# Optimization experiments

Measured on AMD Instinct MI355X. Metric: run time of the kernel, lower is better.

Reference implementation:

```python
import jax, jax.numpy as jnp
import numpy as np

NUM_HEADS = 12
TOP_K = 2
ROPE_THETA = 10000.0
EPS = 1e-6

def _rmsnorm(x, w):
    return x * jax.lax.rsqrt(jnp.mean(x * x, axis=-1, keepdims=True) + EPS) * w

def _rotate_half(t):
    t1, t2 = jnp.split(t, 2, axis=-1)
    return jnp.concatenate([-t2, t1], axis=-1)

def setup_inputs() -> dict:
    key = jax.random.key(0)
    ks = jax.random.split(key, 8)
    B, S, H, E, F = 2, 2048, 768, 8, 3072
    s = 0.02
    return {
        "x": jax.random.normal(ks[0], (B, S, H), dtype=jnp.float32),
        "attn_norm_w": jnp.ones((H,), dtype=jnp.float32),
        "wqkv": jax.random.normal(ks[1], (H, 3 * H), dtype=jnp.float32) * s,
        "wo": jax.random.normal(ks[2], (H, H), dtype=jnp.float32) * s,
        "ffn_norm_w": jnp.ones((H,), dtype=jnp.float32),
        "router_w": jax.random.normal(ks[3], (H, E), dtype=jnp.float32) * s,
        "w1": jax.random.normal(ks[4], (E, H, F), dtype=jnp.float32) * s,
        "w2": jax.random.normal(ks[5], (E, F, H), dtype=jnp.float32) * s,
    }

def reference(x, attn_norm_w, wqkv, wo, ffn_norm_w, router_w, w1, w2):
    B, S, H = x.shape
    NH, Dh = NUM_HEADS, H // NUM_HEADS
    E = router_w.shape[1]

    # ---- attention sub-block: x = x + attn(rmsnorm(x)) ----
    h = _rmsnorm(x, attn_norm_w)
    qkv = h @ wqkv  # (B,S,3H)
    q, k, v = [t.reshape(B, S, NH, Dh) for t in jnp.split(qkv, 3, axis=-1)]

    # RoPE (llama-style half-split rotation)
    half = Dh // 2
    inv_freq = 1.0 / (ROPE_THETA ** (jnp.arange(half, dtype=jnp.float32) / half))
    ang = jnp.arange(S, dtype=jnp.float32)[:, None] * inv_freq[None, :]  # (S, half)
    cos = jnp.concatenate([jnp.cos(ang)] * 2, axis=-1)[None, :, None, :].astype(x.dtype)
    sin = jnp.concatenate([jnp.sin(ang)] * 2, axis=-1)[None, :, None, :].astype(x.dtype)
    q = q * cos + _rotate_half(q) * sin
    k = k * cos + _rotate_half(k) * sin

    scores = jnp.einsum('bqhd,bkhd->bhqk', q, k) / jnp.sqrt(jnp.asarray(Dh, x.dtype))
    causal = jnp.tril(jnp.ones((S, S), dtype=bool))
    scores = jnp.where(causal[None, None], scores, jnp.asarray(-1e9, x.dtype))
    attn = jax.nn.softmax(scores, axis=-1)
    o = jnp.einsum('bhqk,bkhd->bqhd', attn, v).reshape(B, S, H) @ wo
    x = x + o

    # ---- MoE FFN sub-block: x = x + moe(rmsnorm(x)) ----
    hn = _rmsnorm(x, ffn_norm_w).reshape(-1, H)  # (T,H)
    logits = hn @ router_w  # (T,E)
    probs = jax.nn.softmax(logits, axis=-1)
    top_v, top_i = jax.lax.top_k(probs, TOP_K)  # (T,K)
    top_v = top_v / jnp.sum(top_v, axis=-1, keepdims=True)
    onehot = jax.nn.one_hot(top_i, E, dtype=x.dtype)  # (T,K,E)
    combine = jnp.einsum('tke,tk->te', onehot, top_v)  # (T,E)

    h1 = jnp.einsum('th,ehf->etf', hn, w1)
    h2 = jnp.einsum('etf,efh->eth', jax.nn.silu(h1), w2)
    moe_out = jnp.einsum('eth,te->th', h2, combine).reshape(B, S, H)

    # load-balancing aux loss (switch-style)
    frac = jnp.mean(jnp.sum(onehot, axis=1), axis=0) / TOP_K  # (E,)
    mean_prob = jnp.mean(probs, axis=0)  # (E,)
    aux = jnp.asarray(E, x.dtype) * jnp.sum(frac * mean_prob)

    return (x + moe_out, aux)
```

## Files before the change

kernel.cpp:

```cpp
#include <hip/hip_runtime.h>
#include <cstdint>
#include <cstddef>

typedef __bf16 bf16;
typedef bf16 bf16x8 __attribute__((ext_vector_type(8)));
typedef bf16 bf16x4 __attribute__((ext_vector_type(4)));
typedef float f32x4 __attribute__((ext_vector_type(4)));

static constexpr size_t SKS = (size_t)10240 * 768;

template <int N> struct ICst { static constexpr int v = N; };

__device__ __forceinline__ void async_cp16(const void* g, void* l) {
    __builtin_amdgcn_global_load_lds(
        (const __attribute__((address_space(1))) unsigned int*)(unsigned long long)g,
        (__attribute__((address_space(3))) unsigned int*)(unsigned int)(unsigned long long)l,
        16, 0, 0);
}

#define BARX() __builtin_amdgcn_s_barrier()
#define LGKM0() asm volatile("s_waitcnt lgkmcnt(0)" ::: "memory")
#define VMC8() asm volatile("s_waitcnt vmcnt(8)" ::: "memory")
#define VMC0() asm volatile("s_waitcnt vmcnt(0)" ::: "memory")

template <bool NT>
__device__ __forceinline__ void tc_body(const float* __restrict__ in, bf16* __restrict__ out,
                                        int R, int C, int r0, int c0, float* shf) {
    float (*tile)[33] = (float(*)[33])shf;
    int tid = threadIdx.x;
    int lr = tid >> 3, lc = (tid & 7) * 4;
    const f32x4* gp = (const f32x4*)&in[(size_t)(r0 + lr) * C + c0 + lc];
    f32x4 v = NT ? __builtin_nontemporal_load(gp) : *gp;
    tile[lr][lc] = v[0]; tile[lr][lc + 1] = v[1]; tile[lr][lc + 2] = v[2]; tile[lr][lc + 3] = v[3];
    __syncthreads();
    int sc = tid >> 3, sr = (tid & 7) * 4;
    bf16x4 o;
    o[0] = (bf16)tile[sr][sc]; o[1] = (bf16)tile[sr + 1][sc];
    o[2] = (bf16)tile[sr + 2][sc]; o[3] = (bf16)tile[sr + 3][sc];
    bf16* dst = &out[(size_t)(c0 + sc) * R + r0 + sr];
    if (NT) {
        union { bf16x4 b; unsigned long long u; } cv;
        cv.b = o;
        __builtin_nontemporal_store(cv.u, (unsigned long long*)dst);
    } else {
        *(bf16x4*)dst = o;
    }
}

__global__ __launch_bounds__(256) void prep1(const float* __restrict__ x,
                                             const float* __restrict__ anw,
                                             bf16* __restrict__ hbuf,
                                             const float* __restrict__ wqkv,
                                             bf16* __restrict__ wqkvT,
                                             const float* __restrict__ wo,
                                             bf16* __restrict__ woT,
                                             int* __restrict__ ctrl) {
    __shared__ __align__(16) float shf[32 * 33];
    const int bid = (int)blockIdx.x, tid = threadIdx.x;
    if (bid < 4096) {
        const float* xr = x + (size_t)bid * 768;
        float v0 = xr[tid], v1 = xr[tid + 256], v2 = xr[tid + 512];
        float s = v0 * v0 + v1 * v1 + v2 * v2;
#pragma unroll
        for (int off = 32; off; off >>= 1) s += __shfl_xor(s, off, 64);
        if ((tid & 63) == 0) shf[tid >> 6] = s;
        __syncthreads();
        float tot = shf[0] + shf[1] + shf[2] + shf[3];
        float rs = rsqrtf(tot * (1.f / 768.f) + 1e-6f);
        bf16* o = hbuf + (size_t)bid * 768;
        o[tid]       = (bf16)(v0 * rs * anw[tid]);
        o[tid + 256] = (bf16)(v1 * rs * anw[tid + 256]);
        o[tid + 512] = (bf16)(v2 * rs * anw[tid + 512]);
    } else if (bid < 5824) {
        int i = bid - 4096;
        tc_body<false>(wqkv, wqkvT, 768, 2304, (i / 72) * 32, (i % 72) * 32, shf);
    } else if (bid < 6400) {
        int i = bid - 5824;
        tc_body<false>(wo, woT, 768, 768, (i / 24) * 32, (i % 24) * 32, shf);
    } else {
        if (tid < 64) ctrl[tid] = 0;
    }
}

__global__ __launch_bounds__(256) void rope_kernel(const bf16* __restrict__ qkv,
                                                   bf16* __restrict__ qb,
                                                   bf16* __restrict__ kb,
                                                   bf16* __restrict__ vtb) {
    __shared__ float vs[64][65];
    const int tid = threadIdx.x;
    const int s0 = blockIdx.x * 64, bh = blockIdx.y;
    const int b = bh / 12, h = bh - b * 12;
    const float qscale = 0.18033688f;
#pragma unroll
    for (int i = 0; i < 16; ++i) {
        int idx = i * 256 + tid;
        int sl = idx >> 6, d = idx & 63;
        int sg = s0 + sl;
        size_t base = ((size_t)b * 2048 + sg) * 2304;
        float qv = (float)qkv[base + h * 64 + d];
        float kv = (float)qkv[base + 768 + h * 64 + d];
        float vv = (float)qkv[base + 1536 + h * 64 + d];
        float qp = (float)qkv[base + h * 64 + (d ^ 32)];
        float kp = (float)qkv[base + 768 + h * 64 + (d ^ 32)];
        int jj = d & 31;
        float invf = __expf(-(float)jj * (9.210340371976184f / 32.f));
        float ang = (float)sg * invf;
        float cv, sv;
        __sincosf(ang, &sv, &cv);
        float rq = (d < 32) ? -qp : qp;
        float rk = (d < 32) ? -kp : kp;
        qb[((size_t)bh * 2048 + sg) * 64 + d] = (bf16)((qv * cv + rq * sv) * qscale);
        kb[((size_t)bh * 2048 + sg) * 64 + d] = (bf16)(kv * cv + rk * sv);
        vs[sl][d] = vv;
    }
    __syncthreads();
#pragma unroll
    for (int i = 0; i < 16; ++i) {
        int idx = i * 256 + tid;
        int d = idx >> 6, sl = idx & 63;
        vtb[(size_t)bh * 64 * 2048 + (size_t)d * 2048 + s0 + sl] = (bf16)vs[sl][d];
    }
}

struct AttnSh {
    bf16 Qs[2][64][32];
    bf16 Ks[2][2][64][32];
    bf16 Vts[2][2][64][32];
    bf16 Ps[4][1024];
};
union ShU { AttnSh a; float tile[32 * 33]; };

__global__ __launch_bounds__(256) void attn_tw(const bf16* __restrict__ qb,
                                               const bf16* __restrict__ kb,
                                               const bf16* __restrict__ vtb,
                                               bf16* __restrict__ ob,
                                               const float* __restrict__ w1,
                                               bf16* __restrict__ w1T,
                                               const float* __restrict__ w2,
                                               bf16* __restrict__ w2T) {
    __shared__ __align__(16) ShU sh;
    const int bid = (int)blockIdx.x;

    if (bid >= 768) {
        int i = bid - 768;
        if (i < 18432) {
            int bz = i / 2304, r = i - bz * 2304;
            tc_body<true>(w1 + (size_t)bz * 768 * 3072, w1T + (size_t)bz * 768 * 3072,
                          768, 3072, ((r / 96) % 24) * 32, (r % 96) * 32, sh.tile);
        } else {
            i -= 18432;
            int bz = i / 2304, r = i - bz * 2304;
            tc_body<true>(w2 + (size_t)bz * 3072 * 768, w2T + (size_t)bz * 3072 * 768,
                          3072, 768, ((r / 24) % 96) * 32, (r % 24) * 32, sh.tile);
        }
        return;
    }

    __builtin_amdgcn_s_setprio(1);

    const int tid = threadIdx.x, lane = tid & 63, w = tid >> 6;
    const int quad = lane >> 4, l16 = lane & 15;
    const int linear = bid;
    const int xcd = linear & 7, j = linear >> 3;
    const int bh = xcd * 3 + (j >> 5);
    const int qt = 31 - (j & 31);
    const int q0 = qt * 64;
    const int b = bh / 12, h = bh - b * 12;

    const bf16* qhead = qb + (size_t)bh * 2048 * 64;
    const bf16* khead = kb + (size_t)bh * 2048 * 64;
    const bf16* vthead = vtb + (size_t)bh * 64 * 2048;

#pragma unroll
    for (int i = 0; i < 2; ++i) {
        int o = (i * 256 + tid) * 16;
        int kk = o >> 12, row = (o >> 6) & 63, el = (o & 63) >> 1;
        async_cp16(qhead + (size_t)(q0 + row) * 64 + kk * 32 + el,
                   (char*)sh.a.Qs + (size_t)(i * 256 + w * 64) * 16);
    }
    __syncthreads();
    bf16x8 bq[2];
#pragma unroll
    for (int kk = 0; kk < 2; ++kk)
        bq[kk] = *(const bf16x8*)&sh.a.Qs[kk][w * 16 + l16][quad * 8];

    f32x4 o_acc[4] = {};
    float m_st = -1e30f, l_st = 0.f;

    for (int j2 = 0; j2 <= qt; j2 += 2) {
        int nt2 = (j2 + 1 <= qt) ? 2 : 1;
        __syncthreads();
#pragma unroll
        for (int t = 0; t < 2; ++t) {
            if (t >= nt2) break;
            int kv0 = (j2 + t) * 64;
#pragma unroll
            for (int i = 0; i < 2; ++i) {
                int o = (i * 256 + tid) * 16;
                int kk = o >> 12, row = (o >> 6) & 63, el = (o & 63) >> 1;
                async_cp16(khead + (size_t)(kv0 + row) * 64 + kk * 32 + el,
                           (char*)&sh.a.Ks[t] + (size_t)(i * 256 + w * 64) * 16);
                async_cp16(vthead + (size_t)row * 2048 + kv0 + kk * 32 + el,
                           (char*)&sh.a.Vts[t] + (size_t)(i * 256 + w * 64) * 16);
            }
        }
        __syncthreads();

#pragma unroll
        for (int t = 0; t < 2; ++t) {
            if (t >= nt2) break;

            f32x4 sacc[4] = {};
#pragma unroll
            for (int kk = 0; kk < 2; ++kk) {
                bf16x8 ak[4];
#pragma unroll
                for (int ni = 0; ni < 4; ++ni)
                    ak[ni] = *(const bf16x8*)&sh.a.Ks[t][kk][ni * 16 + l16][quad * 8];
#pragma unroll
                for (int ni = 0; ni < 4; ++ni)
                    sacc[ni] = __builtin_amdgcn_mfma_f32_16x16x32_bf16(ak[ni], bq[kk], sacc[ni], 0, 0, 0);
            }

            if (j2 + t == qt) {
                int ql = w * 16 + l16;
#pragma unroll
                for (int ni = 0; ni < 4; ++ni)
#pragma unroll
                    for (int r = 0; r < 4; ++r)
                        if (ni * 16 + quad * 4 + r > ql) sacc[ni][r] = -1e30f;
            }

            float mx = sacc[0][0];
#pragma unroll
            for (int ni = 0; ni < 4; ++ni)
#pragma unroll
                for (int r = 0; r < 4; ++r) mx = fmaxf(mx, sacc[ni][r]);
            mx = fmaxf(mx, __shfl_xor(mx, 16, 64));
            mx = fmaxf(mx, __shfl_xor(mx, 32, 64));
            float mnew = fmaxf(m_st, mx);
            float alpha = exp2f(m_st - mnew);
            m_st = mnew;
            float rsum = 0.f;
#pragma unroll
            for (int ni = 0; ni < 4; ++ni)
#pragma unroll
                for (int r = 0; r < 4; ++r) {
                    float pv = exp2f(sacc[ni][r] - mnew);
                    sacc[ni][r] = pv;
                    rsum += pv;
                }
            rsum += __shfl_xor(rsum, 16, 64);
            rsum += __shfl_xor(rsum, 32, 64);
            l_st = l_st * alpha + rsum;

            float af[4];
#pragma unroll
            for (int r = 0; r < 4; ++r) af[r] = __shfl(alpha, quad * 4 + r, 64);
#pragma unroll
            for (int ni = 0; ni < 4; ++ni)
#pragma unroll
                for (int r = 0; r < 4; ++r) o_acc[ni][r] *= af[r];

            bf16* pb = sh.a.Ps[w];
#pragma unroll
            for (int ni = 0; ni < 4; ++ni)
#pragma unroll
                for (int r = 0; r < 4; ++r) {
                    int kv = ni * 16 + quad * 4 + r;
                    int ch = (kv >> 3) ^ (l16 & 7);
                    pb[l16 * 64 + ch * 8 + (kv & 7)] = (bf16)sacc[ni][r];
                }

#pragma unroll
            for (int kk = 0; kk < 2; ++kk) {
                int ch = (kk * 4 + quad) ^ (l16 & 7);
                bf16x8 ap = *(const bf16x8*)&pb[l16 * 64 + ch * 8];
                bf16x8 bv[4];
#pragma unroll
                for (int ni = 0; ni < 4; ++ni)
                    bv[ni] = *(const bf16x8*)&sh.a.Vts[t][kk][ni * 16 + l16][quad * 8];
#pragma unroll
                for (int ni = 0; ni < 4; ++ni)
                    o_acc[ni] = __builtin_amdgcn_mfma_f32_16x16x32_bf16(ap, bv[ni], o_acc[ni], 0, 0, 0);
            }
        }
    }

    float lf[4];
#pragma unroll
    for (int r = 0; r < 4; ++r) lf[r] = 1.f / __shfl(l_st, quad * 4 + r, 64);
#pragma unroll
    for (int ni = 0; ni < 4; ++ni)
#pragma unroll
        for (int r = 0; r < 4; ++r) {
            int rowg = q0 + w * 16 + quad * 4 + r;
            size_t tk = (size_t)b * 2048 + rowg;
            ob[tk * 768 + h * 64 + ni * 16 + l16] = (bf16)(o_acc[ni][r] * lf[r]);
        }
    __builtin_amdgcn_s_setprio(0);
}

__global__ __launch_bounds__(256) void rms_router(const float* __restrict__ x1,
                                                  const float* __restrict__ w,
                                                  const float* __restrict__ rw,
                                                  bf16* __restrict__ hn,
                                                  int* __restrict__ topi,
                                                  float* __restrict__ topw,
                                                  float* __restrict__ probsb) {
    __shared__ float hnf[768];
    __shared__ float part[256];
    __shared__ float lg[8];
    __shared__ float probs[8];
    __shared__ float red[4];
    int row = blockIdx.x, tid = threadIdx.x;
    const float* xr = x1 + (size_t)row * 768;
    float v0 = xr[tid], v1 = xr[tid + 256], v2 = xr[tid + 512];
    float s = v0 * v0 + v1 * v1 + v2 * v2;
#pragma unroll
    for (int off = 32; off; off >>= 1) s += __shfl_xor(s, off, 64);
    if ((tid & 63) == 0) red[tid >> 6] = s;
    __syncthreads();
    float tot = red[0] + red[1] + red[2] + red[3];
    float rs = rsqrtf(tot * (1.f / 768.f) + 1e-6f);
    float h0 = v0 * rs * w[tid], h1v = v1 * rs * w[tid + 256], h2v = v2 * rs * w[tid + 512];
    hnf[tid] = h0; hnf[tid + 256] = h1v; hnf[tid + 512] = h2v;
    bf16* o = hn + (size_t)row * 768;
    o[tid] = (bf16)h0; o[tid + 256] = (bf16)h1v; o[tid + 512] = (bf16)h2v;
    __syncthreads();
    int e = tid & 7, seg = tid >> 3;
    float p = 0.f;
#pragma unroll
    for (int j = 0; j < 24; ++j) { int k = seg * 24 + j; p += hnf[k] * rw[k * 8 + e]; }
    part[tid] = p;
    __syncthreads();
    if (tid < 8) { float a = 0.f; for (int sgi = 0; sgi < 32; ++sgi) a += part[sgi * 8 + tid]; lg[tid] = a; }
    __syncthreads();
    if (tid == 0) {
        float mx = lg[0];
        for (int i = 1; i < 8; ++i) mx = fmaxf(mx, lg[i]);
        float ssum = 0.f, ex[8];
        for (int i = 0; i < 8; ++i) { ex[i] = __expf(lg[i] - mx); ssum += ex[i]; }
        float inv = 1.f / ssum;
        for (int i = 0; i < 8; ++i) probs[i] = ex[i] * inv;
        int e0 = 0; float p0 = probs[0];
        for (int i = 1; i < 8; ++i) if (probs[i] > p0) { p0 = probs[i]; e0 = i; }
        int e1 = -1; float p1 = -1.f;
        for (int i = 0; i < 8; ++i) if (i != e0 && probs[i] > p1) { p1 = probs[i]; e1 = i; }
        float wsum = p0 + p1;
        topi[row * 2] = e0; topi[row * 2 + 1] = e1;
        topw[row * 2] = p0 / wsum; topw[row * 2 + 1] = p1 / wsum;
    }
    __syncthreads();
    if (tid < 8) probsb[(size_t)row * 8 + tid] = probs[tid];
}

__global__ __launch_bounds__(256) void router_stats(const float* __restrict__ probsb,
                                                    const int* __restrict__ topi,
                                                    int* ctrl, int4* tiles, float* auxOut) {
    __shared__ float pws[4][8];
    __shared__ int cws[4][8];
    int tid = threadIdx.x;
    float s[8] = {};
    int cnt[8] = {};
    for (int t = tid; t < 4096; t += 256) {
        const float4* p = (const float4*)(probsb + (size_t)t * 8);
        float4 a = p[0], b = p[1];
        s[0] += a.x; s[1] += a.y; s[2] += a.z; s[3] += a.w;
        s[4] += b.x; s[5] += b.y; s[6] += b.z; s[7] += b.w;
        int e0 = topi[2 * t], e1 = topi[2 * t + 1];
#pragma unroll
        for (int e = 0; e < 8; ++e) cnt[e] += (e == e0) + (e == e1);
    }
#pragma unroll
    for (int e = 0; e < 8; ++e)
#pragma unroll
        for (int off = 32; off; off >>= 1) {
            s[e] += __shfl_xor(s[e], off, 64);
            cnt[e] += __shfl_xor(cnt[e], off, 64);
        }
    if ((tid & 63) == 0) {
#pragma unroll
        for (int e = 0; e < 8; ++e) { pws[tid >> 6][e] = s[e]; cws[tid >> 6][e] = cnt[e]; }
    }
    __syncthreads();
    if (tid == 0) {
        int off = 0, nt = 0;
        float aux = 0.f;
        for (int e = 0; e < 8; ++e) {
            int ne = cws[0][e] + cws[1][e] + cws[2][e] + cws[3][e];
            float ps = pws[0][e] + pws[1][e] + pws[2][e] + pws[3][e];
            ctrl[e] = ne;
            ctrl[32 + e] = off;
            int ntl = (ne + 255) >> 8;
            for (int i = 0; i < ntl; ++i) { tiles[nt] = make_int4(e, off + i * 256, off + ne, 0); ++nt; }
            off += ntl << 8;
            aux += ((float)ne * (1.f / 8192.f)) * (ps * (1.f / 4096.f));
        }
        ctrl[24] = nt;
        auxOut[0] = 8.f * aux;
    }
}

__global__ __launch_bounds__(256) void place_tokens(const int* __restrict__ topi,
                                                    int* ctrl, int* __restrict__ perm,
                                                    int* __restrict__ tokslot) {
    __shared__ int lcnt[8], lbase[8];
    int tid = threadIdx.x;
    int t = blockIdx.x * 256 + tid;
    if (tid < 8) lcnt[tid] = 0;
    __syncthreads();
    int e0 = topi[2 * t], e1 = topi[2 * t + 1];
    int p0 = atomicAdd(&lcnt[e0], 1);
    int p1 = atomicAdd(&lcnt[e1], 1);
    __syncthreads();
    if (tid < 8) lbase[tid] = atomicAdd(&ctrl[16 + tid], lcnt[tid]);
    __syncthreads();
    int g0 = ctrl[32 + e0] + lbase[e0] + p0;
    int g1 = ctrl[32 + e1] + lbase[e1] + p1;
    perm[g0] = t; perm[g1] = t;
    tokslot[2 * t] = g0; tokslot[2 * t + 1] = g1;
}

__global__ __launch_bounds__(192) void moe_combine(const float* __restrict__ h2p,
                                                   const int* __restrict__ tokslot,
                                                   const float* __restrict__ topw,
                                                   float* __restrict__ out) {
    int t = blockIdx.x, tid = threadIdx.x;
    int s0 = tokslot[2 * t], s1 = tokslot[2 * t + 1];
    float w0 = topw[2 * t], w1 = topw[2 * t + 1];
    int c = tid * 4;
    float4 a0 = *(const float4*)(h2p + (size_t)s0 * 768 + c);
    float4 a1 = *(const float4*)(h2p + SKS + (size_t)s0 * 768 + c);
    float4 b0 = *(const float4*)(h2p + (size_t)s1 * 768 + c);
    float4 b1 = *(const float4*)(h2p + SKS + (size_t)s1 * 768 + c);
    float4* o = (float4*)(out + (size_t)t * 768 + c);
    float4 ov = *o;
    ov.x += w0 * (a0.x + a1.x) + w1 * (b0.x + b1.x);
    ov.y += w0 * (a0.y + a1.y) + w1 * (b0.y + b1.y);
    ov.z += w0 * (a0.z + a1.z) + w1 * (b0.z + b1.z);
    ov.w += w0 * (a0.w + a1.w) + w1 * (b0.w + b1.w);
    *o = ov;
}

template <int MODE, int KTOT, int SK>
__global__ __launch_bounds__(512, 2) void gemm8p(const bf16* __restrict__ A,
                                                 const bf16* __restrict__ Bt,
                                                 int N,
                                                 bf16* __restrict__ outB,
                                                 float* __restrict__ outF,
                                                 const int4* __restrict__ tiles,
                                                 const int* __restrict__ ctrl,
                                                 const int* __restrict__ perm) {
    constexpr int KB = KTOT / SK;
    constexpr int nT = KB >> 6;
    __shared__ __align__(16) bf16 As[2][2][128 * 64];
    __shared__ __align__(16) bf16 Bs[2][2][128 * 64];
    __shared__ int sPerm[256];

    const int tid = threadIdx.x, lane = tid & 63, wid = tid >> 6;
    const int wr = wid >> 2, wc = wid & 3;
    const int quad = lane >> 4, l16 = lane & 15;

    const int NB = N >> 8;
    const int nwg = (int)gridDim.x, q8 = nwg >> 3;
    const int L = (int)blockIdx.x;
    const int lin = (L & 7) * q8 + (L >> 3);
    int mt, nb, sk = 0;
    if (SK == 2) { int d = NB * 2; mt = lin / d; int r = lin - mt * d; nb = r >> 1; sk = r & 1; }
    else         { mt = lin / NB; nb = lin - mt * NB; }
    const int n0 = nb << 8;
    const int k0 = sk * KB;

    int m0 = 0, row0 = 0;
    if (MODE == 0) {
        m0 = mt << 8;
    } else {
        if (mt >= ctrl[24]) return;
        int4 td = tiles[mt];
        row0 = td.y;
        Bt += (size_t)td.x * (size_t)N * KTOT;
        if (MODE == 2) {
            if (tid < 256) {
                int g = row0 + tid;
                sPerm[tid] = perm[(g < td.z) ? g : row0];
            }
            __syncthreads();
        }
    }

    const int r0t = tid >> 3, s0t = tid & 7;
    const int cOff = ((s0t ^ (r0t & 7)) << 3);
    unsigned aOff[2][2], bOff[2][2];
#pragma unroll
    for (int h = 0; h < 2; ++h)
#pragma unroll
        for (int i = 0; i < 2; ++i) {
            int rrow = h * 128 + i * 64 + r0t;
            bOff[h][i] = (unsigned)((((n0 + rrow) * KTOT) + k0 + cOff) * 2);
            int ar = (MODE == 0) ? (m0 + rrow) : (MODE == 2 ? sPerm[rrow] : row0 + rrow);
            aOff[h][i] = (unsigned)(((ar * KTOT) + k0 + cOff) * 2);
        }
    const char* Ab = (const char*)A;
    const char* Bb = (const char*)Bt;

    auto stA = [&](int buf, int ktB) {
#pragma unroll
        for (int h = 0; h < 2; ++h)
#pragma unroll
            for (int i = 0; i < 2; ++i)
                async_cp16(Ab + aOff[h][i] + ktB,
                           (char*)As[buf][h] + (size_t)((i * 512 + wid * 64) * 16));
    };
    auto stB = [&](int buf, int ktB) {
#pragma unroll
        for (int h = 0; h < 2; ++h)
#pragma unroll
            for (int i = 0; i < 2; ++i)
                async_cp16(Bb + bOff[h][i] + ktB,
                           (char*)Bs[buf][h] + (size_t)((i * 512 + wid * 64) * 16));
    };

    const bf16* aP[2][2];
    const bf16* bP[2][2];
#pragma unroll
    for (int bb = 0; bb < 2; ++bb)
#pragma unroll
        for (int kk = 0; kk < 2; ++kk) {
            int swz = ((kk * 4 + quad) ^ (l16 & 7)) * 8;
            aP[bb][kk] = (const bf16*)As[bb][wr] + l16 * 64 + swz;
            bP[bb][kk] = (const bf16*)Bs[bb][wc >> 1] + ((wc & 1) * 64 + l16) * 64 + swz;
        }

    f32x4 acc[8][4] = {};
    bf16x8 aLo[4][2], aHi[4][2], bLo[2][2], bHi[2][2];

    stA(0, 0); stB(0, 0); stA(1, 128); stB(1, 128);
    VMC8();
    BARX();

    auto dotile = [&](auto BC, int t) {
        constexpr int b = decltype(BC)::v;
        const bool st = (t + 2 < nT);
        const int ktB = (t + 2) << 7;

#pragma unroll
        for (int mi = 0; mi < 4; ++mi) {
            aLo[mi][0] = *(const bf16x8*)(aP[b][0] + mi * 1024);
            aLo[mi][1] = *(const bf16x8*)(aP[b][1] + mi * 1024);
        }
#pragma unroll
        for (int ni = 0; ni < 2; ++ni) {
            bLo[ni][0] = *(const bf16x8*)(bP[b][0] + ni * 1024);
            bLo[ni][1] = *(const bf16x8*)(bP[b][1] + ni * 1024);
        }
        BARX(); LGKM0();
        __builtin_amdgcn_s_setprio(1);
#pragma unroll
        for (int mi = 0; mi < 4; ++mi)
#pragma unroll
            for (int ni = 0; ni < 2; ++ni) {
                acc[mi][ni] = __builtin_amdgcn_mfma_f32_16x16x32_bf16(aLo[mi][0], bLo[ni][0], acc[mi][ni], 0, 0, 0);
                acc[mi][ni] = __builtin_amdgcn_mfma_f32_16x16x32_bf16(aLo[mi][1], bLo[ni][1], acc[mi][ni], 0, 0, 0);
            }
        __builtin_amdgcn_s_setprio(0);
        BARX();

#pragma unroll
        for (int ni = 0; ni < 2; ++ni) {
            bHi[ni][0] = *(const bf16x8*)(bP[b][0] + (ni + 2) * 1024);
            bHi[ni][1] = *(const bf16x8*)(bP[b][1] + (ni + 2) * 1024);
        }
        BARX(); LGKM0();
        __builtin_amdgcn_s_setprio(1);
#pragma unroll
        for (int mi = 0; mi < 4; ++mi)
#pragma unroll
            for (int ni = 0; ni < 2; ++ni) {
                acc[mi][ni + 2] = __builtin_amdgcn_mfma_f32_16x16x32_bf16(aLo[mi][0], bHi[ni][0], acc[mi][ni + 2], 0, 0, 0);
                acc[mi][ni + 2] = __builtin_amdgcn_mfma_f32_16x16x32_bf16(aLo[mi][1], bHi[ni][1], acc[mi][ni + 2], 0, 0, 0);
            }
        __builtin_amdgcn_s_setprio(0);
        BARX();

#pragma unroll
        for (int mi = 0; mi < 4; ++mi) {
            aHi[mi][0] = *(const bf16x8*)(aP[b][0] + (mi + 4) * 1024);
            aHi[mi][1] = *(const bf16x8*)(aP[b][1] + (mi + 4) * 1024);
        }
        if (st) stB(b, ktB);
        BARX(); LGKM0();
        __builtin_amdgcn_s_setprio(1);
#pragma unroll
        for (int mi = 0; mi < 4; ++mi)
#pragma unroll
            for (int ni = 0; ni < 2; ++ni) {
                acc[mi + 4][ni + 2] = __builtin_amdgcn_mfma_f32_16x16x32_bf16(aHi[mi][0], bHi[ni][0], acc[mi + 4][ni + 2], 0, 0, 0);
                acc[mi + 4][ni + 2] = __builtin_amdgcn_mfma_f32_16x16x32_bf16(aHi[mi][1], bHi[ni][1], acc[mi + 4][ni + 2], 0, 0, 0);
            }
        __builtin_amdgcn_s_setprio(0);
        BARX();

        if (st) stA(b, ktB);
        BARX();
        __builtin_amdgcn_s_setprio(1);
#pragma unroll
        for (int mi = 0; mi < 4; ++mi)
#pragma unroll
            for (int ni = 0; ni < 2; ++ni) {
                acc[mi + 4][ni] = __builtin_amdgcn_mfma_f32_16x16x32_bf16(aHi[mi][0], bLo[ni][0], acc[mi + 4][ni], 0, 0, 0);
                acc[mi + 4][ni] = __builtin_amdgcn_mfma_f32_16x16x32_bf16(aHi[mi][1], bLo[ni][1], acc[mi + 4][ni], 0, 0, 0);
            }
        __builtin_amdgcn_s_setprio(0);
        if (st) { VMC8(); } else if (t + 2 == nT) { VMC0(); }
        BARX();
    };

    for (int t = 0; t < nT; t += 2) {
        dotile(ICst<0>{}, t);
        dotile(ICst<1>{}, t + 1);
    }

#pragma unroll
    for (int mi = 0; mi < 8; ++mi)
#pragma unroll
        for (int ni = 0; ni < 4; ++ni)
#pragma unroll
            for (int r = 0; r < 4; ++r) {
                int lrow = wr * 128 + mi * 16 + quad * 4 + r;
                int col  = n0 + wc * 64 + ni * 16 + l16;
                float v = acc[mi][ni][r];
                if (MODE == 0) {
                    outB[(size_t)(m0 + lrow) * N + col] = (bf16)v;
                } else if (MODE == 2) {
                    float sv = v / (1.f + __expf(-v));
                    outB[(size_t)(row0 + lrow) * N + col] = (bf16)sv;
                } else {
                    outF[(size_t)sk * SKS + (size_t)(row0 + lrow) * N + col] = v;
                }
            }
}

template <int MODE, int NBX, int MTX>
__global__ __launch_bounds__(256) void gemm_nt(const bf16* __restrict__ A,
                                               const bf16* __restrict__ Bt,
                                               int N, int K,
                                               const float* __restrict__ xres,
                                               float* __restrict__ outF,
                                               bf16* __restrict__ outB) {
    __shared__ __align__(16) bf16 As[2][128 * 32];
    __shared__ __align__(16) bf16 Bs[2][128 * 32];

    const int tid = threadIdx.x, lane = tid & 63, w = tid >> 6;
    const int wr = w >> 1, wc = w & 1, quad = lane >> 4, l16 = lane & 15;

    const int L = blockIdx.x;
    const int xcd = L & 7, j = L >> 3;
    const int mt = xcd * MTX + j / NBX;
    const int n0 = (j % NBX) * 128;
    const int m0 = mt * 128;

    auto stage = [&](int buf, int kt) {
#pragma unroll
        for (int i = 0; i < 2; ++i) {
            int c = i * 256 + tid;
            int r = c >> 2, koff = (c & 3) * 8;
            async_cp16(A + (size_t)(m0 + r) * K + kt + koff,
                       (char*)As[buf] + (size_t)(i * 256 + w * 64) * 16);
            async_cp16(Bt + (size_t)(n0 + r) * K + kt + koff,
                       (char*)Bs[buf] + (size_t)(i * 256 + w * 64) * 16);
        }
    };

    f32x4 acc[4][4] = {};
    const int nIt = K >> 5;
    stage(0, 0);

    for (int it = 0; it < nIt; ++it) {
        const int cur = it & 1;
        __syncthreads();
        if (it + 1 < nIt) stage(cur ^ 1, (it + 1) << 5);

        bf16x8 af[4], bfr[4];
#pragma unroll
        for (int mi = 0; mi < 4; ++mi)
            af[mi] = *(const bf16x8*)(As[cur] + (wr * 64 + mi * 16 + l16) * 32 + quad * 8);
#pragma unroll
        for (int ni = 0; ni < 4; ++ni)
            bfr[ni] = *(const bf16x8*)(Bs[cur] + (wc * 64 + ni * 16 + l16) * 32 + quad * 8);
#pragma unroll
        for (int mi = 0; mi < 4; ++mi)
#pragma unroll
            for (int ni = 0; ni < 4; ++ni)
                acc[mi][ni] = __builtin_amdgcn_mfma_f32_16x16x32_bf16(af[mi], bfr[ni], acc[mi][ni], 0, 0, 0);
    }

#pragma unroll
    for (int mi = 0; mi < 4; ++mi)
#pragma unroll
        for (int ni = 0; ni < 4; ++ni)
#pragma unroll
            for (int r = 0; r < 4; ++r) {
                int lrow = wr * 64 + mi * 16 + quad * 4 + r;
                int col = n0 + wc * 64 + ni * 16 + l16;
                float v = acc[mi][ni][r];
                if (MODE == 1) {
                    size_t idx = (size_t)(m0 + lrow) * N + col;
                    outF[idx] = v + xres[idx];
                } else {
                    outB[(size_t)(m0 + lrow) * N + col] = (bf16)v;
                }
            }
}

extern "C" void kernel_launch(void* const* d_in, const int* in_sizes, int n_in,
                              void* d_out, int out_size, void* d_ws, size_t ws_size,
                              hipStream_t stream) {
    const float* x    = (const float*)d_in[0];
    const float* anw  = (const float*)d_in[1];
    const float* wqkv = (const float*)d_in[2];
    const float* wo   = (const float*)d_in[3];
    const float* fnw  = (const float*)d_in[4];
    const float* rw   = (const float*)d_in[5];
    const float* w1   = (const float*)d_in[6];
    const float* w2   = (const float*)d_in[7];
    float* out = (float*)d_out;

    char* ws = (char*)d_ws;
    size_t off = 0;
    auto alloc = [&](size_t bytes) -> char* {
        char* p = ws + off;
        off = (off + bytes + 255) & ~(size_t)255;
        return p;
    };
    bf16* wqkvT = (bf16*)alloc(2304ull * 768 * 2);
    bf16* woT   = (bf16*)alloc(768ull * 768 * 2);
    bf16* w2T   = (bf16*)alloc(8ull * 768 * 3072 * 2);
    bf16* w1T   = (bf16*)alloc(8ull * 3072 * 768 * 2);
    bf16* hbuf  = (bf16*)alloc(4096ull * 768 * 2);
    bf16* qkvb  = (bf16*)alloc(4096ull * 2304 * 2);
    bf16* qb    = (bf16*)alloc(24ull * 2048 * 64 * 2);
    bf16* kb    = (bf16*)alloc(24ull * 2048 * 64 * 2);
    bf16* vtb   = (bf16*)alloc(24ull * 64 * 2048 * 2);
    bf16* obuf  = (bf16*)alloc(4096ull * 768 * 2);
    bf16* hn    = (bf16*)alloc(4096ull * 768 * 2);
    int*  topi  = (int*)alloc(4096ull * 2 * 4);
    float* topw = (float*)alloc(4096ull * 2 * 4);
    float* probsb = (float*)alloc(4096ull * 8 * 4);
    int*  ctrl  = (int*)alloc(64 * 4);
    int4* tiles = (int4*)alloc(80 * 16);
    int*  perm  = (int*)alloc(10240 * 4);
    int*  tokslot = (int*)alloc(4096ull * 2 * 4);
    bf16* h1    = (bf16*)alloc(10240ull * 3072 * 2);
    float* h2p  = (float*)w1T;
    (void)ws_size; (void)in_sizes; (void)n_in;

    prep1<<<6401, 256, 0, stream>>>(x, anw, hbuf, wqkv, wqkvT, wo, woT, ctrl);
    gemm8p<0, 768, 1><<<144, 512, 0, stream>>>(hbuf, wqkvT, 2304, qkvb, nullptr,
                                               nullptr, nullptr, nullptr);
    rope_kernel<<<dim3(32, 24), 256, 0, stream>>>(qkvb, qb, kb, vtb);
    attn_tw<<<768 + 36864, 256, 0, stream>>>(qb, kb, vtb, obuf, w1, w1T, w2, w2T);
    gemm_nt<1, 6, 4><<<192, 256, 0, stream>>>(obuf, woT, 768, 768, x, out, nullptr);
    rms_router<<<4096, 256, 0, stream>>>(out, fnw, rw, hn, topi, topw, probsb);
    router_stats<<<1, 256, 0, stream>>>(probsb, topi, ctrl, tiles, out + (out_size - 1));
    place_tokens<<<16, 256, 0, stream>>>(topi, ctrl, perm, tokslot);
    gemm8p<2, 768, 1><<<480, 512, 0, stream>>>(hn, w1T, 3072, h1, nullptr,
                                               tiles, ctrl, perm);
    gemm8p<3, 3072, 2><<<240, 512, 0, stream>>>(h1, w2T, 768, nullptr, h2p,
                                                tiles, ctrl, perm);
    moe_combine<<<4096, 192, 0, stream>>>(h2p, tokslot, topw, out);
}
```

Measured before the change: 453.1 us.

## Fuse MoE combine into down-projection GEMM epilogue via weighted atomic adds

The split-K down-projection GEMM now scales each result by its routing weight and atomically adds it straight into the output rows, indexed by token permutation. This removes the fp32 partial buffer and the separate combine kernel. Padding slots are zeroed so they add nothing. In exchange it issues many scattered fp32 atomics to global memory and makes the summation order nondeterministic.

```diff
diff --git a/kernel.cpp b/kernel.cpp
--- a/kernel.cpp
+++ b/kernel.cpp
@@ -23,28 +23,21 @@
 #define VMC8() asm volatile("s_waitcnt vmcnt(8)" ::: "memory")
 #define VMC0() asm volatile("s_waitcnt vmcnt(0)" ::: "memory")
 
-template <bool NT>
+template <bool NTLD>
 __device__ __forceinline__ void tc_body(const float* __restrict__ in, bf16* __restrict__ out,
                                         int R, int C, int r0, int c0, float* shf) {
     float (*tile)[33] = (float(*)[33])shf;
     int tid = threadIdx.x;
     int lr = tid >> 3, lc = (tid & 7) * 4;
     const f32x4* gp = (const f32x4*)&in[(size_t)(r0 + lr) * C + c0 + lc];
-    f32x4 v = NT ? __builtin_nontemporal_load(gp) : *gp;
+    f32x4 v = NTLD ? __builtin_nontemporal_load(gp) : *gp;
     tile[lr][lc] = v[0]; tile[lr][lc + 1] = v[1]; tile[lr][lc + 2] = v[2]; tile[lr][lc + 3] = v[3];
     __syncthreads();
     int sc = tid >> 3, sr = (tid & 7) * 4;
     bf16x4 o;
     o[0] = (bf16)tile[sr][sc]; o[1] = (bf16)tile[sr + 1][sc];
     o[2] = (bf16)tile[sr + 2][sc]; o[3] = (bf16)tile[sr + 3][sc];
-    bf16* dst = &out[(size_t)(c0 + sc) * R + r0 + sr];
-    if (NT) {
-        union { bf16x4 b; unsigned long long u; } cv;
-        cv.b = o;
-        __builtin_nontemporal_store(cv.u, (unsigned long long*)dst);
-    } else {
-        *(bf16x4*)dst = o;
-    }
+    *(bf16x4*)&out[(size_t)(c0 + sc) * R + r0 + sr] = o;
 }
 
 __global__ __launch_bounds__(256) void prep1(const float* __restrict__ x,
@@ -54,7 +47,9 @@
                                              bf16* __restrict__ wqkvT,
                                              const float* __restrict__ wo,
                                              bf16* __restrict__ woT,
-                                             int* __restrict__ ctrl) {
+                                             int* __restrict__ ctrl,
+                                             int* __restrict__ perm,
+                                             float* __restrict__ slotw) {
     __shared__ __align__(16) float shf[32 * 33];
     const int bid = (int)blockIdx.x, tid = threadIdx.x;
     if (bid < 4096) {
@@ -79,6 +74,7 @@
         tc_body<false>(wo, woT, 768, 768, (i / 24) * 32, (i % 24) * 32, shf);
     } else {
         if (tid < 64) ctrl[tid] = 0;
+        for (int i = tid; i < 10240; i += 256) { perm[i] = 0; slotw[i] = 0.f; }
     }
 }
 
@@ -403,8 +399,9 @@
 }
 
 __global__ __launch_bounds__(256) void place_tokens(const int* __restrict__ topi,
+                                                    const float* __restrict__ topw,
                                                     int* ctrl, int* __restrict__ perm,
-                                                    int* __restrict__ tokslot) {
+                                                    float* __restrict__ slotw) {
     __shared__ int lcnt[8], lbase[8];
     int tid = threadIdx.x;
     int t = blockIdx.x * 256 + tid;
@@ -419,28 +416,7 @@
     int g0 = ctrl[32 + e0] + lbase[e0] + p0;
     int g1 = ctrl[32 + e1] + lbase[e1] + p1;
     perm[g0] = t; perm[g1] = t;
-    tokslot[2 * t] = g0; tokslot[2 * t + 1] = g1;
-}
-
-__global__ __launch_bounds__(192) void moe_combine(const float* __restrict__ h2p,
-                                                   const int* __restrict__ tokslot,
-                                                   const float* __restrict__ topw,
-                                                   float* __restrict__ out) {
-    int t = blockIdx.x, tid = threadIdx.x;
-    int s0 = tokslot[2 * t], s1 = tokslot[2 * t + 1];
-    float w0 = topw[2 * t], w1 = topw[2 * t + 1];
-    int c = tid * 4;
-    float4 a0 = *(const float4*)(h2p + (size_t)s0 * 768 + c);
-    float4 a1 = *(const float4*)(h2p + SKS + (size_t)s0 * 768 + c);
-    float4 b0 = *(const float4*)(h2p + (size_t)s1 * 768 + c);
-    float4 b1 = *(const float4*)(h2p + SKS + (size_t)s1 * 768 + c);
-    float4* o = (float4*)(out + (size_t)t * 768 + c);
-    float4 ov = *o;
-    ov.x += w0 * (a0.x + a1.x) + w1 * (b0.x + b1.x);
-    ov.y += w0 * (a0.y + a1.y) + w1 * (b0.y + b1.y);
-    ov.z += w0 * (a0.z + a1.z) + w1 * (b0.z + b1.z);
-    ov.w += w0 * (a0.w + a1.w) + w1 * (b0.w + b1.w);
-    *o = ov;
+    slotw[g0] = topw[2 * t]; slotw[g1] = topw[2 * t + 1];
 }
 
 template <int MODE, int KTOT, int SK>
@@ -451,7 +427,8 @@
                                                  float* __restrict__ outF,
                                                  const int4* __restrict__ tiles,
                                                  const int* __restrict__ ctrl,
-                                                 const int* __restrict__ perm) {
+                                                 const int* __restrict__ perm,
+                                                 const float* __restrict__ slotw) {
     constexpr int KB = KTOT / SK;
     constexpr int nT = KB >> 6;
     __shared__ __align__(16) bf16 As[2][2][128 * 64];
@@ -636,7 +613,8 @@
                     float sv = v / (1.f + __expf(-v));
                     outB[(size_t)(row0 + lrow) * N + col] = (bf16)sv;
                 } else {
-                    outF[(size_t)sk * SKS + (size_t)(row0 + lrow) * N + col] = v;
+                    int s = row0 + lrow;
+                    atomicAdd(&outF[(size_t)perm[s] * N + col], v * slotw[s]);
                 }
             }
 }
@@ -750,23 +728,21 @@
     int*  ctrl  = (int*)alloc(64 * 4);
     int4* tiles = (int4*)alloc(80 * 16);
     int*  perm  = (int*)alloc(10240 * 4);
-    int*  tokslot = (int*)alloc(4096ull * 2 * 4);
+    float* slotw = (float*)alloc(10240 * 4);
     bf16* h1    = (bf16*)alloc(10240ull * 3072 * 2);
-    float* h2p  = (float*)w1T;
-    (void)ws_size; (void)in_sizes; (void)n_in;
-
-    prep1<<<6401, 256, 0, stream>>>(x, anw, hbuf, wqkv, wqkvT, wo, woT, ctrl);
+    (void)ws_size; (void)in_sizes; (void)n_in; (void)SKS;
+
+    prep1<<<6401, 256, 0, stream>>>(x, anw, hbuf, wqkv, wqkvT, wo, woT, ctrl, perm, slotw);
     gemm8p<0, 768, 1><<<144, 512, 0, stream>>>(hbuf, wqkvT, 2304, qkvb, nullptr,
-                                               nullptr, nullptr, nullptr);
+                                               nullptr, nullptr, nullptr, nullptr);
     rope_kernel<<<dim3(32, 24), 256, 0, stream>>>(qkvb, qb, kb, vtb);
     attn_tw<<<768 + 36864, 256, 0, stream>>>(qb, kb, vtb, obuf, w1, w1T, w2, w2T);
     gemm_nt<1, 6, 4><<<192, 256, 0, stream>>>(obuf, woT, 768, 768, x, out, nullptr);
     rms_router<<<4096, 256, 0, stream>>>(out, fnw, rw, hn, topi, topw, probsb);
     router_stats<<<1, 256, 0, stream>>>(probsb, topi, ctrl, tiles, out + (out_size - 1));
-    place_tokens<<<16, 256, 0, stream>>>(topi, ctrl, perm, tokslot);
+    place_tokens<<<16, 256, 0, stream>>>(topi, topw, ctrl, perm, slotw);
     gemm8p<2, 768, 1><<<480, 512, 0, stream>>>(hn, w1T, 3072, h1, nullptr,
-                                               tiles, ctrl, perm);
-    gemm8p<3, 3072, 2><<<240, 512, 0, stream>>>(h1, w2T, 768, nullptr, h2p,
-                                                tiles, ctrl, perm);
-    moe_combine<<<4096, 192, 0, stream>>>(h2p, tokslot, topw, out);
-}
+                                               tiles, ctrl, perm, nullptr);
+    gemm8p<3, 3072, 2><<<240, 512, 0, stream>>>(h1, w2T, 768, nullptr, out,
+                                                tiles, ctrl, perm, slotw);
+}
```

Measured after the change: 707.5 us. +56.2%, slower.
